# Optimization experiments

Measured on AMD Instinct MI355X. Metric: run time of the kernel, lower is better.

## Reference

```python
import jax, jax.numpy as jnp
import numpy as np

B, N, C, K = 8, 4096, 128, 20  # batch, points-per-cloud, channels (n_cout), knn neighbors
NEG_SLOPE = 0.01  # torch F.leaky_relu default


def setup_inputs() -> dict:
    key = jax.random.key(0)
    ks = jax.random.split(key, 6)
    s = 1.0 / np.sqrt(C).astype(np.float32)
    xyz = jax.random.normal(ks[0], (B, 3, N), jnp.float32)
    points = jax.random.normal(ks[1], (B, C, N), jnp.float32)
    Wc = jax.random.normal(ks[2], (C, C), jnp.float32) * s  # center 1x1 conv weight (out,in)
    bc = jax.random.normal(ks[3], (C,), jnp.float32) * s
    Wg = jax.random.normal(ks[4], (C, C), jnp.float32) * s  # grouped 1x1 conv weight
    bg = jax.random.normal(ks[5], (C,), jnp.float32) * s
    return {"xyz": xyz, "points": points, "Wc": Wc, "bc": bc, "Wg": Wg, "bg": bg}


def reference(xyz, points, Wc, bc, Wg, bg):
    # xyz: [B,3,N], points: [B,C,N]
    k = K
    shortcut = points
    p = jax.nn.leaky_relu(points, NEG_SLOPE)        # [B,C,N]
    pt = jnp.transpose(p, (0, 2, 1))                # [B,N,C]
    xt = jnp.transpose(xyz, (0, 2, 1))              # [B,N,3]

    # pairwise squared distances [B,N,N]
    sq_norm = jnp.sum(xt * xt, axis=-1)             # [B,N]
    sq = sq_norm[:, :, None] - 2.0 * jnp.einsum('bnd,bmd->bnm', xt, xt) + sq_norm[:, None, :]

    # knn: k+1 nearest (incl. self), drop self -> [B,N,k]
    _, idx = jax.lax.top_k(-sq, k + 1)
    idx = idx[:, :, 1:]

    # gather neighbor features: [B,N,k,C]
    grouped = jax.vmap(lambda a, i: a[i])(pt, idx)

    # center 1x1 conv on [B,C,1,N] == per-point linear
    center = jnp.einsum('oc,bcn->bon', Wc, p) + bc[None, :, None]      # [B,C,N]
    # grouped 1x1 conv on [B,C,k,N]
    gout = jnp.einsum('oc,bnkc->bokn', Wg, grouped) + bg[None, :, None, None]  # [B,C,k,N]

    # mean over concat([center(1), grouped(k)], axis=2) then residual
    pooled = (center + jnp.sum(gout, axis=2)) / (k + 1)
    return pooled + shortcut
```

## Files before the change

### kernel.cpp

```cpp
#include <hip/hip_runtime.h>

#define B 8
#define N 4096
#define C 128
#define C2 256
#define KNN 21
#define CAP 22

typedef unsigned long long u64;
typedef unsigned int u32;
typedef unsigned short u16;

typedef __attribute__((ext_vector_type(8))) short bf16x8;
typedef __attribute__((ext_vector_type(4))) float f32x4;

__device__ __forceinline__ float bf2f(u16 u) {
    return __uint_as_float(((u32)u) << 16);
}
__device__ __forceinline__ u16 f2bf(float f) {
    u32 x = __float_as_uint(f);
    return (u16)((x + 0x7FFFu + ((x >> 16) & 1u)) >> 16);
}

__global__ __launch_bounds__(256) void k_transpose_lrelu(
        const float* __restrict__ pts, u16* __restrict__ X) {
    __shared__ u16 tile[32][33];
    int b  = blockIdx.z;
    int c0 = blockIdx.y * 32;
    int n0 = blockIdx.x * 32;
    int tx = threadIdx.x, ty = threadIdx.y;
    const float* src = pts + (size_t)b * C * N;
    #pragma unroll
    for (int i = 0; i < 32; i += 8) {
        float v = src[(size_t)(c0 + ty + i) * N + n0 + tx];
        if (v < 0.f) v = __fmul_rn(v, 0.01f);
        tile[ty + i][tx] = f2bf(v);
    }
    __syncthreads();
    u16* dst = X + (size_t)b * N * C2;
    #pragma unroll
    for (int i = 0; i < 32; i += 8) {
        dst[(size_t)(n0 + ty + i) * C2 + (c0 + tx)] = tile[tx][ty + i];
    }
}

__global__ __launch_bounds__(256) void k_knn_gather(
        const float* __restrict__ xyz, u16* __restrict__ X) {
    __shared__ __align__(16) char lds[50176];
    float4* stg  = (float4*)lds;
    u32*    kbuf = (u32*)(lds + 16384);
    u16*    ibuf = (u16*)(lds + 16384 + 22528);
    u64*    mg   = (u64*)lds;
    __shared__ u16 win[64 * KNN];

    int tid = threadIdx.x;
    int w = tid >> 6, l = tid & 63;
    int b = blockIdx.y;
    int n0 = blockIdx.x * 64;
    int nq = n0 + l;

    const float* xz = xyz + (size_t)b * 3 * N;
    float qx = xz[nq], qy = xz[N + nq], qz = xz[2 * N + nq];
    float snq = __fadd_rn(__fadd_rn(__fmul_rn(qx, qx), __fmul_rn(qy, qy)),
                          __fmul_rn(qz, qz));

    u32 key[KNN], idx[KNN];
    #pragma unroll
    for (int i = 0; i < KNN; ++i) { key[i] = 0xFFFFFFFFu; idx[i] = 0u; }
    int cnt = 0;
    u32 thr = 0xFFFFFFFFu;
    float4* mystg = stg + w * 256;

    auto compact = [&]() {
        #pragma unroll 1
        for (int i = 0; i < CAP; ++i) {
            if (__ballot(i < cnt) == 0ull) break;
            u32 kv = kbuf[i * 256 + tid];
            u32 iv = ibuf[i * 256 + tid];
            bool ins = (i < cnt) && (kv < key[20]);
            if (__ballot(ins) != 0ull) {
                key[20] = ins ? kv : key[20];
                idx[20] = ins ? iv : idx[20];
                #pragma unroll
                for (int t = 19; t >= 0; --t) {
                    bool sw = key[t] > key[t + 1];
                    u32 ka = sw ? key[t + 1] : key[t];
                    u32 kz = sw ? key[t] : key[t + 1];
                    u32 ia = sw ? idx[t + 1] : idx[t];
                    u32 iz = sw ? idx[t] : idx[t + 1];
                    key[t] = ka; key[t + 1] = kz;
                    idx[t] = ia; idx[t + 1] = iz;
                }
            }
        }
        cnt = 0;
        thr = key[20];
    };

    for (int sc = 0; sc < 4; ++sc) {
        int m0 = w * 1024 + sc * 256;
        #pragma unroll
        for (int r = 0; r < 4; ++r) {
            int j = l + 64 * r, m = m0 + j;
            float x = xz[m], y = xz[N + m], z = xz[2 * N + m];
            float sn = __fadd_rn(__fadd_rn(__fmul_rn(x, x), __fmul_rn(y, y)),
                                 __fmul_rn(z, z));
            mystg[j] = make_float4(x, y, z, sn);
        }
        asm volatile("s_waitcnt lgkmcnt(0)" ::: "memory");
        for (int cc = 0; cc < 256; cc += 8) {
            #pragma unroll
            for (int j = 0; j < 8; ++j) {
                float4 cp = mystg[cc + j];
                int m = m0 + cc + j;
                float dot = __fadd_rn(__fadd_rn(__fmul_rn(qx, cp.x),
                                                __fmul_rn(qy, cp.y)),
                                      __fmul_rn(qz, cp.z));
                float sq = __fadd_rn(__fsub_rn(snq, __fadd_rn(dot, dot)), cp.w);
                u32 bits = __float_as_uint(sq);
                u32 kb = bits ^ (0x80000000u | (u32)(((int)bits) >> 31));
                kbuf[cnt * 256 + tid] = kb;
                ibuf[cnt * 256 + tid] = (u16)m;
                cnt += (kb < thr);
            }
            if (__ballot(cnt >= 15) != 0ull) compact();
        }
    }
    compact();

    __syncthreads();
    #pragma unroll
    for (int j = 0; j < KNN; ++j)
        mg[(w * 64 + l) * KNN + j] = ((u64)key[j] << 32) | (u64)idx[j];
    __syncthreads();

    if (w == 0) {
        int p0 = 0, p1 = 0, p2 = 0, p3 = 0;
        for (int j = 0; j < KNN; ++j) {
            u64 c0 = mg[(0 * 64 + l) * KNN + p0];
            u64 c1 = mg[(1 * 64 + l) * KNN + p1];
            u64 c2 = mg[(2 * 64 + l) * KNN + p2];
            u64 c3 = mg[(3 * 64 + l) * KNN + p3];
            u64 m01 = c0 < c1 ? c0 : c1; int s01 = c0 < c1 ? 0 : 1;
            u64 m23 = c2 < c3 ? c2 : c3; int s23 = c2 < c3 ? 2 : 3;
            u64 mm = m01 < m23 ? m01 : m23;
            int sel = m01 < m23 ? s01 : s23;
            win[l * KNN + j] = (u16)(mm & 0xFFFFu);
            p0 += (sel == 0); p1 += (sel == 1); p2 += (sel == 2); p3 += (sel == 3);
        }
    }
    __syncthreads();

    const u16* Xb = X + (size_t)b * N * C2;
    for (int qq = 0; qq < 16; ++qq) {
        int q = w * 16 + qq;
        float f0 = 0.f, f1 = 0.f;
        #pragma unroll
        for (int j = 1; j < KNN; ++j) {
            int m = win[q * KNN + j];
            u32 u2 = *(const u32*)(Xb + (size_t)m * C2 + 2 * l);
            f0 += bf2f((u16)(u2 & 0xFFFFu));
            f1 += bf2f((u16)(u2 >> 16));
        }
        u16* dst = X + ((size_t)b * N + n0 + q) * C2 + 128 + 2 * l;
        *(u32*)dst = ((u32)f2bf(f1) << 16) | (u32)f2bf(f0);
    }
}

__global__ __launch_bounds__(256) void k_gemm_mfma(
        const u16* __restrict__ X, const float* __restrict__ Wc,
        const float* __restrict__ Wg, const float* __restrict__ pts,
        const float* __restrict__ bc, const float* __restrict__ bg,
        float* __restrict__ out) {
    int wid = blockIdx.x * 4 + (threadIdx.x >> 6);
    int lane = threadIdx.x & 63;
    int ot = wid & 7;
    int nt = wid >> 3;
    int b  = nt >> 6;
    int n0 = (nt & 63) * 64;

    int l16 = lane & 15, lq = lane >> 4;
    const u16* Xb = X + (size_t)b * N * C2;
    const u16* bptr0 = Xb + (size_t)(n0 + 0 * 16 + l16) * C2 + lq * 8;
    const u16* bptr1 = Xb + (size_t)(n0 + 1 * 16 + l16) * C2 + lq * 8;
    const u16* bptr2 = Xb + (size_t)(n0 + 2 * 16 + l16) * C2 + lq * 8;
    const u16* bptr3 = Xb + (size_t)(n0 + 3 * 16 + l16) * C2 + lq * 8;
    const float* wrowc = Wc + (size_t)(ot * 16 + l16) * 128 + lq * 8;
    const float* wrowg = Wg + (size_t)(ot * 16 + l16) * 128 + lq * 8;

    f32x4 acc0 = {0.f, 0.f, 0.f, 0.f};
    f32x4 acc1 = {0.f, 0.f, 0.f, 0.f};
    f32x4 acc2 = {0.f, 0.f, 0.f, 0.f};
    f32x4 acc3 = {0.f, 0.f, 0.f, 0.f};
    #pragma unroll
    for (int kk = 0; kk < 8; ++kk) {
        const float* ws = (kk < 4) ? (wrowc + kk * 32) : (wrowg + (kk - 4) * 32);
        float4 wa = *(const float4*)ws;
        float4 wb = *(const float4*)(ws + 4);
        bf16x8 a;
        a[0] = (short)f2bf(wa.x); a[1] = (short)f2bf(wa.y);
        a[2] = (short)f2bf(wa.z); a[3] = (short)f2bf(wa.w);
        a[4] = (short)f2bf(wb.x); a[5] = (short)f2bf(wb.y);
        a[6] = (short)f2bf(wb.z); a[7] = (short)f2bf(wb.w);
        bf16x8 b0 = *(const bf16x8*)(bptr0 + kk * 32);
        bf16x8 b1 = *(const bf16x8*)(bptr1 + kk * 32);
        bf16x8 b2 = *(const bf16x8*)(bptr2 + kk * 32);
        bf16x8 b3 = *(const bf16x8*)(bptr3 + kk * 32);
        acc0 = __builtin_amdgcn_mfma_f32_16x16x32_bf16(a, b0, acc0, 0, 0, 0);
        acc1 = __builtin_amdgcn_mfma_f32_16x16x32_bf16(a, b1, acc1, 0, 0, 0);
        acc2 = __builtin_amdgcn_mfma_f32_16x16x32_bf16(a, b2, acc2, 0, 0, 0);
        acc3 = __builtin_amdgcn_mfma_f32_16x16x32_bf16(a, b3, acc3, 0, 0, 0);
    }

    const float inv21 = 1.0f / 21.0f;
    float bias[4];
    #pragma unroll
    for (int r = 0; r < 4; ++r) {
        int o = ot * 16 + lq * 4 + r;
        bias[r] = bc[o] + 20.f * bg[o];
    }
    const float* pb = pts + (size_t)b * C * N;
    float* ob = out + (size_t)b * C * N;
    f32x4 accs[4] = {acc0, acc1, acc2, acc3};
    #pragma unroll
    for (int t = 0; t < 4; ++t) {
        int n = n0 + t * 16 + l16;
        #pragma unroll
        for (int r = 0; r < 4; ++r) {
            int o = ot * 16 + lq * 4 + r;
            ob[(size_t)o * N + n] =
                (accs[t][r] + bias[r]) * inv21 + pb[(size_t)o * N + n];
        }
    }
}

extern "C" void kernel_launch(void* const* d_in, const int* in_sizes, int n_in,
                              void* d_out, int out_size, void* d_ws, size_t ws_size,
                              hipStream_t stream) {
    const float* xyz = (const float*)d_in[0];
    const float* pts = (const float*)d_in[1];
    const float* Wc  = (const float*)d_in[2];
    const float* bc  = (const float*)d_in[3];
    const float* Wg  = (const float*)d_in[4];
    const float* bg  = (const float*)d_in[5];
    float* out = (float*)d_out;

    u16* X = (u16*)d_ws;

    k_transpose_lrelu<<<dim3(N / 32, C / 32, B), dim3(32, 8), 0, stream>>>(pts, X);
    k_knn_gather<<<dim3(N / 64, B), dim3(256), 0, stream>>>(xyz, X);
    k_gemm_mfma<<<dim3(1024), dim3(256), 0, stream>>>(X, Wc, Wg, pts, bc, bg, out);
}
```

Measured before the change: 285.7 us.

## Split each KNN query across eight threads and merge eight partial top-k lists

The KNN kernel now handles 32 queries per block instead of 64. Each query's candidate scan is split across two lanes in each of the four waves, so each thread scans 512 points rather than 1024, and the launch grid doubles. The final merge becomes an 8-way merge over split key and index arrays. Candidate buffer capacity and the compaction threshold are reduced, which shrinks LDS use and may raise occupancy. In exchange, the merge is longer, more top-k lists have to be maintained and compacted, and gather work per block is smaller.

```diff
diff --git a/kernel.cpp b/kernel.cpp
--- a/kernel.cpp
+++ b/kernel.cpp
@@ -5,7 +5,7 @@
 #define C 128
 #define C2 256
 #define KNN 21
-#define CAP 22
+#define CAP 12
 
 typedef unsigned long long u64;
 typedef unsigned int u32;
@@ -46,18 +46,20 @@
 
 __global__ __launch_bounds__(256) void k_knn_gather(
         const float* __restrict__ xyz, u16* __restrict__ X) {
-    __shared__ __align__(16) char lds[50176];
+    __shared__ __align__(16) char lds[34816];
     float4* stg  = (float4*)lds;
     u32*    kbuf = (u32*)(lds + 16384);
-    u16*    ibuf = (u16*)(lds + 16384 + 22528);
-    u64*    mg   = (u64*)lds;
-    __shared__ u16 win[64 * KNN];
+    u16*    ibuf = (u16*)(lds + 16384 + 12288);
+    u32*    mk   = (u32*)lds;
+    u16*    mi   = (u16*)(lds + 21504);
+    __shared__ u16 win[32 * KNN];
 
     int tid = threadIdx.x;
     int w = tid >> 6, l = tid & 63;
+    int q = l >> 1, h = l & 1;
     int b = blockIdx.y;
-    int n0 = blockIdx.x * 64;
-    int nq = n0 + l;
+    int n0 = blockIdx.x * 32;
+    int nq = n0 + q;
 
     const float* xz = xyz + (size_t)b * 3 * N;
     float qx = xz[nq], qy = xz[N + nq], qz = xz[2 * N + nq];
@@ -69,7 +71,6 @@
     for (int i = 0; i < KNN; ++i) { key[i] = 0xFFFFFFFFu; idx[i] = 0u; }
     int cnt = 0;
     u32 thr = 0xFFFFFFFFu;
-    float4* mystg = stg + w * 256;
 
     auto compact = [&]() {
         #pragma unroll 1
@@ -98,21 +99,24 @@
     };
 
     for (int sc = 0; sc < 4; ++sc) {
-        int m0 = w * 1024 + sc * 256;
         #pragma unroll
         for (int r = 0; r < 4; ++r) {
-            int j = l + 64 * r, m = m0 + j;
+            int e = l + 64 * r;
+            int he = e >> 7, je = e & 127;
+            int m = w * 1024 + he * 512 + sc * 128 + je;
             float x = xz[m], y = xz[N + m], z = xz[2 * N + m];
             float sn = __fadd_rn(__fadd_rn(__fmul_rn(x, x), __fmul_rn(y, y)),
                                  __fmul_rn(z, z));
-            mystg[j] = make_float4(x, y, z, sn);
+            stg[w * 256 + e] = make_float4(x, y, z, sn);
         }
         asm volatile("s_waitcnt lgkmcnt(0)" ::: "memory");
-        for (int cc = 0; cc < 256; cc += 8) {
+        int mbase = w * 1024 + h * 512 + sc * 128;
+        const float4* mystg = stg + w * 256 + h * 128;
+        for (int cc = 0; cc < 128; cc += 4) {
             #pragma unroll
-            for (int j = 0; j < 8; ++j) {
-                float4 cp = mystg[cc + j];
-                int m = m0 + cc + j;
+            for (int u = 0; u < 4; ++u) {
+                float4 cp = mystg[cc + u];
+                int m = mbase + cc + u;
                 float dot = __fadd_rn(__fadd_rn(__fmul_rn(qx, cp.x),
                                                 __fmul_rn(qy, cp.y)),
                                       __fmul_rn(qz, cp.z));
@@ -123,46 +127,57 @@
                 ibuf[cnt * 256 + tid] = (u16)m;
                 cnt += (kb < thr);
             }
-            if (__ballot(cnt >= 15) != 0ull) compact();
+            if (__ballot(cnt > 8) != 0ull) compact();
         }
     }
     compact();
 
     __syncthreads();
     #pragma unroll
-    for (int j = 0; j < KNN; ++j)
-        mg[(w * 64 + l) * KNN + j] = ((u64)key[j] << 32) | (u64)idx[j];
-    __syncthreads();
-
-    if (w == 0) {
-        int p0 = 0, p1 = 0, p2 = 0, p3 = 0;
+    for (int j = 0; j < KNN; ++j) {
+        mk[(w * 64 + l) * KNN + j] = key[j];
+        mi[(w * 64 + l) * KNN + j] = idx[j];
+    }
+    __syncthreads();
+
+    if (w == 0 && l < 32) {
+        int p[1];
+        int p0 = 0, p1 = 0, p2 = 0, p3 = 0, p4 = 0, p5 = 0, p6 = 0, p7 = 0;
+        (void)p;
+        #pragma unroll 1
         for (int j = 0; j < KNN; ++j) {
-            u64 c0 = mg[(0 * 64 + l) * KNN + p0];
-            u64 c1 = mg[(1 * 64 + l) * KNN + p1];
-            u64 c2 = mg[(2 * 64 + l) * KNN + p2];
-            u64 c3 = mg[(3 * 64 + l) * KNN + p3];
+            #define LOADC(r, pr) \
+                u64 c##r = ((u64)mk[(((r) >> 1) * 64 + l * 2 + ((r) & 1)) * KNN + pr] << 16) \
+                         |  (u64)mi[(((r) >> 1) * 64 + l * 2 + ((r) & 1)) * KNN + pr];
+            LOADC(0, p0) LOADC(1, p1) LOADC(2, p2) LOADC(3, p3)
+            LOADC(4, p4) LOADC(5, p5) LOADC(6, p6) LOADC(7, p7)
+            #undef LOADC
             u64 m01 = c0 < c1 ? c0 : c1; int s01 = c0 < c1 ? 0 : 1;
             u64 m23 = c2 < c3 ? c2 : c3; int s23 = c2 < c3 ? 2 : 3;
-            u64 mm = m01 < m23 ? m01 : m23;
-            int sel = m01 < m23 ? s01 : s23;
+            u64 m45 = c4 < c5 ? c4 : c5; int s45 = c4 < c5 ? 4 : 5;
+            u64 m67 = c6 < c7 ? c6 : c7; int s67 = c6 < c7 ? 6 : 7;
+            u64 m03 = m01 < m23 ? m01 : m23; int s03 = m01 < m23 ? s01 : s23;
+            u64 m47 = m45 < m67 ? m45 : m67; int s47 = m45 < m67 ? s45 : s67;
+            u64 mm  = m03 < m47 ? m03 : m47; int sel = m03 < m47 ? s03 : s47;
             win[l * KNN + j] = (u16)(mm & 0xFFFFu);
             p0 += (sel == 0); p1 += (sel == 1); p2 += (sel == 2); p3 += (sel == 3);
+            p4 += (sel == 4); p5 += (sel == 5); p6 += (sel == 6); p7 += (sel == 7);
         }
     }
     __syncthreads();
 
     const u16* Xb = X + (size_t)b * N * C2;
-    for (int qq = 0; qq < 16; ++qq) {
-        int q = w * 16 + qq;
+    for (int qq = 0; qq < 8; ++qq) {
+        int qg = w * 8 + qq;
         float f0 = 0.f, f1 = 0.f;
         #pragma unroll
         for (int j = 1; j < KNN; ++j) {
-            int m = win[q * KNN + j];
+            int m = win[qg * KNN + j];
             u32 u2 = *(const u32*)(Xb + (size_t)m * C2 + 2 * l);
             f0 += bf2f((u16)(u2 & 0xFFFFu));
             f1 += bf2f((u16)(u2 >> 16));
         }
-        u16* dst = X + ((size_t)b * N + n0 + q) * C2 + 128 + 2 * l;
+        u16* dst = X + ((size_t)b * N + n0 + qg) * C2 + 128 + 2 * l;
         *(u32*)dst = ((u32)f2bf(f1) << 16) | (u32)f2bf(f0);
     }
 }
@@ -248,6 +263,6 @@
     u16* X = (u16*)d_ws;
 
     k_transpose_lrelu<<<dim3(N / 32, C / 32, B), dim3(32, 8), 0, stream>>>(pts, X);
-    k_knn_gather<<<dim3(N / 64, B), dim3(256), 0, stream>>>(xyz, X);
+    k_knn_gather<<<dim3(N / 32, B), dim3(256), 0, stream>>>(xyz, X);
     k_gemm_mfma<<<dim3(1024), dim3(256), 0, stream>>>(X, Wc, Wg, pts, bc, bg, out);
 }
```

Measured after the change: 321.6 us. 12.5% more time.
